# Kernel tuning notes

Hardware: AMD Instinct MI355X
Metric: run time of the kernel (lower is better)

The kernel has to match this reference:

```python
import jax, jax.numpy as jnp
from jax import lax
import numpy as np

C = 16          # channels
K = 3           # deformable kernel size
PAD = 1


def conv3(x, w, b):
    # 3x3 SAME conv, NCHW / OIHW
    y = lax.conv_general_dilated(x, w, (1, 1), 'SAME',
                                 dimension_numbers=('NCHW', 'OIHW', 'NCHW'))
    return y + b[None, :, None, None]


def deform_conv2d(x, offsets, mask, w, b):
    """torchvision-style modulated deformable conv, stride=1, pad=1, dil=1.
    x: [B,C,H,W]; offsets: [B,2*K*K,H,W] (per-tap y,x interleaved);
    mask: [B,K*K,H,W]; w: [Cout,C,K,K]; b: [Cout]."""
    B, Cin, H, W = x.shape
    ky, kx = jnp.meshgrid(jnp.arange(K), jnp.arange(K), indexing='ij')
    ky = ky.reshape(-1).astype(x.dtype)   # [9]
    kx = kx.reshape(-1).astype(x.dtype)
    off = offsets.reshape(B, K * K, 2, H, W)  # off[:,k,0]=dy, off[:,k,1]=dx
    hh = jnp.arange(H, dtype=x.dtype)
    ww = jnp.arange(W, dtype=x.dtype)
    py = hh[None, None, :, None] + (ky - PAD)[None, :, None, None] + off[:, :, 0]  # [B,9,H,W]
    px = ww[None, None, None, :] + (kx - PAD)[None, :, None, None] + off[:, :, 1]
    y0 = jnp.floor(py)
    x0 = jnp.floor(px)
    dy = py - y0
    dx = px - x0

    def sample_one(img, y0b, x0b, dyb, dxb):
        # img [C,H,W]; y0b/x0b/dyb/dxb [9,H,W]
        y0i = y0b.astype(jnp.int32)
        x0i = x0b.astype(jnp.int32)

        def gather(yi, xi):
            valid = ((yi >= 0) & (yi < H) & (xi >= 0) & (xi < W)).astype(img.dtype)
            yc = jnp.clip(yi, 0, H - 1)
            xc = jnp.clip(xi, 0, W - 1)
            return img[:, yc, xc] * valid[None]   # [C,9,H,W]

        v00 = gather(y0i,     x0i)
        v01 = gather(y0i,     x0i + 1)
        v10 = gather(y0i + 1, x0i)
        v11 = gather(y0i + 1, x0i + 1)
        return (v00 * (1 - dyb) * (1 - dxb) + v01 * (1 - dyb) * dxb
                + v10 * dyb * (1 - dxb) + v11 * dyb * dxb)   # [C,9,H,W]

    sampled = jax.vmap(sample_one)(x, y0, x0, dy, dx)          # [B,C,9,H,W]
    sampled = sampled * mask[:, None]                           # modulate
    out = jnp.einsum('bckhw,ock->bohw', sampled, w.reshape(w.shape[0], Cin, K * K))
    return out + b[None, :, None, None]


def setup_inputs() -> dict:
    key = jax.random.key(0)
    ks = iter(jax.random.split(key, 32))

    def w(shape, scale=0.1):
        return (jax.random.normal(next(ks), shape, dtype=jnp.float32) * scale)

    B, H, W = 4, 256, 256
    d = {
        'f_E': jax.random.normal(next(ks), (B, C, H, W), dtype=jnp.float32),
        'f_F': jax.random.normal(next(ks), (B, C, H, W), dtype=jnp.float32),
        # SpatialAttentionBlock
        'sab_att_w1': w((C, 2 * C, 3, 3)), 'sab_att_b1': w((C,)),
        'sab_att_w2': w((1, C, 3, 3)),      'sab_att_b2': w((1,)),
        'sab_ref_w':  w((C, 2 * C, 3, 3)),  'sab_ref_b':  w((C,)),
        # DeformableConvLayer offset/mask net (last layer small -> modest offsets)
        'om_w1': w((C, 2 * C, 3, 3)),       'om_b1': w((C,)),
        'om_w2': w((C, C, 3, 3)),           'om_b2': w((C,)),
        'om_w3': w((3 * K * K, C, 3, 3), 0.05), 'om_b3': w((3 * K * K,), 0.05),
        # deformable conv weight/bias
        'dcb_w': w((C, C, 3, 3)),           'dcb_b': w((C,)),
        # refinements
        'dcbref_w': w((C, 2 * C, 3, 3)),    'dcbref_b': w((C,)),
        'fin_w':    w((C, 2 * C, 3, 3)),    'fin_b':    w((C,)),
    }
    return d


def reference(f_E, f_F,
              sab_att_w1, sab_att_b1, sab_att_w2, sab_att_b2,
              sab_ref_w, sab_ref_b,
              om_w1, om_b1, om_w2, om_b2, om_w3, om_b3,
              dcb_w, dcb_b, dcbref_w, dcbref_b, fin_w, fin_b):
    relu = jax.nn.relu
    # --- SAB branch: sab(f_E, f_F) ---
    comb = jnp.concatenate([f_E, f_F], axis=1)
    M_E = jax.nn.sigmoid(conv3(relu(conv3(comb, sab_att_w1, sab_att_b1)),
                               sab_att_w2, sab_att_b2))          # [B,1,H,W]
    f_Esa = f_E * M_E
    f_EFsa = relu(conv3(jnp.concatenate([f_Esa, f_F], axis=1), sab_ref_w, sab_ref_b))
    # --- DCB branch: dcb_layer(f_F, f_E) -> deform on f_E, cat([f_E, f_F]) ---
    comb2 = jnp.concatenate([f_E, f_F], axis=1)
    om = conv3(relu(conv3(relu(conv3(comb2, om_w1, om_b1)), om_w2, om_b2)),
               om_w3, om_b3)                                      # [B,27,H,W]
    offsets = om[:, :2 * K * K]
    mask = jax.nn.sigmoid(om[:, 2 * K * K:])
    f_Edc = relu(deform_conv2d(f_E, offsets, mask, dcb_w, dcb_b))
    f_EFdc = relu(conv3(jnp.concatenate([f_Edc, f_F], axis=1), dcbref_w, dcbref_b))
    # --- final fusion ---
    f_EF = relu(conv3(jnp.concatenate([f_EFsa, f_EFdc], axis=1), fin_w, fin_b))
    return f_EF
```

## Files before the change

kernel.cpp:

```cpp
#include <hip/hip_runtime.h>
#include <cstdint>
#include <cstddef>

#define HH 256
#define WW 256
#define HWW (HH * WW)

typedef __attribute__((ext_vector_type(8))) short bf16x8;
typedef __attribute__((ext_vector_type(4))) float f32x4;

__device__ inline unsigned short f2bf(float f) {
  unsigned u = __float_as_uint(f);
  unsigned r = (u + 0x7fffu + ((u >> 16) & 1u)) >> 16;
  return (unsigned short)r;
}
__device__ inline float bf2f(unsigned short u) {
  return __uint_as_float((unsigned)u << 16);
}
__device__ inline float bf_lo(unsigned w) { return __uint_as_float(w << 16); }
__device__ inline float bf_hi(unsigned w) { return __uint_as_float(w & 0xffff0000u); }

struct RD { const float* src; void* dst; int cin, cout, mode; };
struct RA { RD d[9]; };

__device__ void repack_one(const RD& t) {
  if (t.mode == 2) {
    const int NST = (t.cin * 9 + 31) / 32;
    const int OT = (t.cout + 15) / 16;
    const int n = OT * NST * 512;
    unsigned short* dst = (unsigned short*)t.dst;
    for (int i = threadIdx.x; i < n; i += 256) {
      int j = i & 7;
      int l = (i >> 3) & 63;
      int rest = i >> 9;
      int s = rest % NST;
      int ot = rest / NST;
      int o = ot * 16 + (l & 15);
      int klin = s * 32 + ((l >> 4) << 3) + j;
      int tap = klin / t.cin;
      int c = klin % t.cin;
      float v = 0.f;
      if (tap < 9 && o < t.cout) v = t.src[(o * t.cin + c) * 9 + tap];
      dst[i] = f2bf(v);
    }
  } else {
    float* dst = (float*)t.dst;
    const int n = t.cin * t.cout * 9;
    for (int i = threadIdx.x; i < n; i += 256) {
      int k = i % 9;
      int rest = i / 9;
      int c = rest % t.cin;
      int o = rest / t.cin;
      if (t.mode == 0) dst[(c * 9 + k) * t.cout + o] = t.src[(o * t.cin + c) * 9 + k];
      else             dst[(k * t.cin + c) * t.cout + o] = t.src[(o * t.cin + c) * 9 + k];
    }
  }
}

__global__ __launch_bounds__(256) void prep_k(
    RA ra, const float* __restrict__ fe, const float* __restrict__ ff,
    unsigned short* __restrict__ xe, unsigned short* __restrict__ xf) {
  const int b = blockIdx.z;
  if (blockIdx.x == 256) {
    const int d0 = b * 3;
    for (int d = d0; d < d0 + 3 && d < 9; ++d) repack_one(ra.d[d]);
    return;
  }
  const int pixel = blockIdx.x * 256 + threadIdx.x;
#pragma unroll
  for (int t = 0; t < 2; ++t) {
    const float* src = t ? ff : fe;
    unsigned short* dst = t ? xf : xe;
    unsigned w[8];
#pragma unroll
    for (int j = 0; j < 8; ++j) {
      unsigned short lo = f2bf(src[((size_t)b * 16 + 2 * j) * HWW + pixel]);
      unsigned short hi = f2bf(src[((size_t)b * 16 + 2 * j + 1) * HWW + pixel]);
      w[j] = (unsigned)lo | ((unsigned)hi << 16);
    }
    uint4* d4 = (uint4*)(dst + ((size_t)b * HWW + pixel) * 16);
    d4[0] = make_uint4(w[0], w[1], w[2], w[3]);
    d4[1] = make_uint4(w[4], w[5], w[6], w[7]);
  }
}

__global__ __launch_bounds__(256) void conv_dual_k(
    const unsigned short* __restrict__ inA, const unsigned short* __restrict__ inB,
    const unsigned short* __restrict__ w1, const float* __restrict__ b1,
    const unsigned short* __restrict__ w2, const float* __restrict__ b2,
    unsigned short* __restrict__ out1, unsigned short* __restrict__ out2) {
  constexpr int NSLOT = 4, NST = 9, SHIFT = 1, STRIDE = 64, PX = 34, PY = 10;
  __shared__ __align__(16) char smem[PY * PX * STRIDE];

  const int b = blockIdx.z;
  const int tx0 = blockIdx.x * 32;
  const int ty0 = blockIdx.y * 8;
  const int tid = threadIdx.x;
  const int lane = tid & 63;
  const int wv = tid >> 6;

  bf16x8 afr1[NST], afr2[NST];
#pragma unroll
  for (int s = 0; s < NST; ++s) {
    afr1[s] = *(const bf16x8*)(w1 + (size_t)((s * 64 + lane) * 8));
    afr2[s] = *(const bf16x8*)(w2 + (size_t)((s * 64 + lane) * 8));
  }

  const int px_l = lane & 15;
  const int og = lane >> 4;

  f32x4 acc1[4], acc2[4];
  {
    f32x4 bv1, bv2;
#pragma unroll
    for (int r = 0; r < 4; ++r) {
      bv1[r] = b1[og * 4 + r];
      bv2[r] = b2[og * 4 + r];
    }
#pragma unroll
    for (int t = 0; t < 4; ++t) { acc1[t] = bv1; acc2[t] = bv2; }
  }

  for (int i = tid; i < PY * PX * NSLOT; i += 256) {
    int pp = i / NSLOT;
    int s = i - pp * NSLOT;
    int ly = pp / PX;
    int lx = pp - ly * PX;
    int gy = ty0 + ly - 1;
    int gx = tx0 + lx - 1;
    uint4 v = make_uint4(0, 0, 0, 0);
    if (gy >= 0 && gy < HH && gx >= 0 && gx < WW) {
      const unsigned short* src = (s < 2) ? inA : inB;
      int sl = (s >= 2) ? s - 2 : s;
      v = *(const uint4*)(src + ((size_t)b * HWW + (size_t)gy * WW + gx) * 16 + sl * 8);
    }
    int swz = (s ^ (pp >> SHIFT)) & 3;
    *(uint4*)(smem + (size_t)pp * STRIDE + (swz << 4)) = v;
  }
  __syncthreads();

  int dpix[NST], dslot[NST];
#pragma unroll
  for (int s = 0; s < NST; ++s) {
    int klin = s * 32 + og * 8;
    int tap = klin / 32;
    int coff = klin % 32;
    dpix[s] = (tap / 3) * PX + (tap % 3);
    dslot[s] = coff >> 3;
  }

  const int oy_l = wv * 2;
#pragma unroll
  for (int t = 0; t < 4; ++t) {
    const int base_pix = (oy_l + (t >> 1)) * PX + (t & 1) * 16 + px_l;
#pragma unroll
    for (int s = 0; s < NST; ++s) {
      int pp = base_pix + dpix[s];
      int off = pp * STRIDE + (((dslot[s] ^ (pp >> SHIFT)) & 3) << 4);
      bf16x8 bvv = *(const bf16x8*)(smem + off);
      acc1[t] = __builtin_amdgcn_mfma_f32_16x16x32_bf16(afr1[s], bvv, acc1[t], 0, 0, 0);
      acc2[t] = __builtin_amdgcn_mfma_f32_16x16x32_bf16(afr2[s], bvv, acc2[t], 0, 0, 0);
    }
  }

#pragma unroll
  for (int t = 0; t < 4; ++t) {
    const int gy = ty0 + oy_l + (t >> 1);
    const int gx = tx0 + (t & 1) * 16 + px_l;
    const size_t base = ((size_t)b * HWW + (size_t)gy * WW + gx) * 16 + og * 4;
    {
      unsigned lo = (unsigned)f2bf(fmaxf(acc1[t][0], 0.f)) |
                    ((unsigned)f2bf(fmaxf(acc1[t][1], 0.f)) << 16);
      unsigned hi = (unsigned)f2bf(fmaxf(acc1[t][2], 0.f)) |
                    ((unsigned)f2bf(fmaxf(acc1[t][3], 0.f)) << 16);
      *(uint2*)(out1 + base) = make_uint2(lo, hi);
    }
    {
      unsigned lo = (unsigned)f2bf(fmaxf(acc2[t][0], 0.f)) |
                    ((unsigned)f2bf(fmaxf(acc2[t][1], 0.f)) << 16);
      unsigned hi = (unsigned)f2bf(fmaxf(acc2[t][2], 0.f)) |
                    ((unsigned)f2bf(fmaxf(acc2[t][3], 0.f)) << 16);
      *(uint2*)(out2 + base) = make_uint2(lo, hi);
    }
  }
}

__global__ __launch_bounds__(256) void sagate_k(
    const unsigned short* __restrict__ xa, const unsigned short* __restrict__ xe,
    const unsigned short* __restrict__ xf,
    const float* __restrict__ gw, const float* __restrict__ gb,
    const unsigned short* __restrict__ wtm, const float* __restrict__ bias,
    unsigned short* __restrict__ out) {
  constexpr int NST = 9, SHIFT = 1, STRIDE = 64, PX = 34, PY = 10;
  __shared__ __align__(16) char smem[PY * PX * STRIDE];

  const int b = blockIdx.z;
  const int tx0 = blockIdx.x * 32;
  const int ty0 = blockIdx.y * 8;
  const int tid = threadIdx.x;
  const int lane = tid & 63;
  const int wv = tid >> 6;

  bf16x8 afr[NST];
#pragma unroll
  for (int s = 0; s < NST; ++s)
    afr[s] = *(const bf16x8*)(wtm + (size_t)((s * 64 + lane) * 8));

  const int px_l = lane & 15;
  const int og = lane >> 4;

  f32x4 acc[4];
  {
    f32x4 bv;
#pragma unroll
    for (int r = 0; r < 4; ++r) bv[r] = bias[og * 4 + r];
#pragma unroll
    for (int t = 0; t < 4; ++t) acc[t] = bv;
  }

  for (int i = tid; i < PY * PX * 2; i += 256) {
    int pp = i >> 1;
    int s = 2 + (i & 1);
    int ly = pp / PX;
    int lx = pp - ly * PX;
    int gy = ty0 + ly - 1;
    int gx = tx0 + lx - 1;
    uint4 v = make_uint4(0, 0, 0, 0);
    if (gy >= 0 && gy < HH && gx >= 0 && gx < WW)
      v = *(const uint4*)(xf + ((size_t)b * HWW + (size_t)gy * WW + gx) * 16 + (s - 2) * 8);
    int swz = (s ^ (pp >> SHIFT)) & 3;
    *(uint4*)(smem + (size_t)pp * STRIDE + (swz << 4)) = v;
  }

  const float gbias = gb[0];
  for (int i = tid; i < PY * PX; i += 256) {
    int ly = i / PX;
    int lx = i - ly * PX;
    int gy = ty0 + ly - 1;
    int gx = tx0 + lx - 1;
    uint4 v0 = make_uint4(0, 0, 0, 0), v1 = make_uint4(0, 0, 0, 0);
    if (gy >= 0 && gy < HH && gx >= 0 && gx < WW) {
      float a = gbias;
#pragma unroll
      for (int ky = 0; ky < 3; ++ky) {
        int ay = gy + ky - 1;
        if (ay < 0 || ay >= HH) continue;
#pragma unroll
        for (int kx = 0; kx < 3; ++kx) {
          int ax = gx + kx - 1;
          if (ax < 0 || ax >= WW) continue;
          const int k = ky * 3 + kx;
          const uint4* p = (const uint4*)(xa + ((size_t)b * HWW + (size_t)ay * WW + ax) * 16);
          uint4 t0 = p[0], t1 = p[1];
          unsigned wv8[8] = {t0.x, t0.y, t0.z, t0.w, t1.x, t1.y, t1.z, t1.w};
#pragma unroll
          for (int j = 0; j < 8; ++j) {
            a = fmaf(bf_lo(wv8[j]), gw[(2 * j) * 9 + k], a);
            a = fmaf(bf_hi(wv8[j]), gw[(2 * j + 1) * 9 + k], a);
          }
        }
      }
      float m = 1.0f / (1.0f + expf(-a));
      const uint4* pe = (const uint4*)(xe + ((size_t)b * HWW + (size_t)gy * WW + gx) * 16);
      uint4 e0 = pe[0], e1 = pe[1];
      unsigned ev[8] = {e0.x, e0.y, e0.z, e0.w, e1.x, e1.y, e1.z, e1.w};
      unsigned r[8];
#pragma unroll
      for (int j = 0; j < 8; ++j) {
        unsigned short lo = f2bf(bf_lo(ev[j]) * m);
        unsigned short hi = f2bf(bf_hi(ev[j]) * m);
        r[j] = (unsigned)lo | ((unsigned)hi << 16);
      }
      v0 = make_uint4(r[0], r[1], r[2], r[3]);
      v1 = make_uint4(r[4], r[5], r[6], r[7]);
    }
    int swz0 = (0 ^ (i >> SHIFT)) & 3;
    int swz1 = (1 ^ (i >> SHIFT)) & 3;
    *(uint4*)(smem + (size_t)i * STRIDE + (swz0 << 4)) = v0;
    *(uint4*)(smem + (size_t)i * STRIDE + (swz1 << 4)) = v1;
  }
  __syncthreads();

  int dpix[NST], dslot[NST];
#pragma unroll
  for (int s = 0; s < NST; ++s) {
    int klin = s * 32 + og * 8;
    int tap = klin / 32;
    int coff = klin % 32;
    dpix[s] = (tap / 3) * PX + (tap % 3);
    dslot[s] = coff >> 3;
  }

  const int oy_l = wv * 2;
#pragma unroll
  for (int t = 0; t < 4; ++t) {
    const int base_pix = (oy_l + (t >> 1)) * PX + (t & 1) * 16 + px_l;
#pragma unroll
    for (int s = 0; s < NST; ++s) {
      int pp = base_pix + dpix[s];
      int off = pp * STRIDE + (((dslot[s] ^ (pp >> SHIFT)) & 3) << 4);
      bf16x8 bvv = *(const bf16x8*)(smem + off);
      acc[t] = __builtin_amdgcn_mfma_f32_16x16x32_bf16(afr[s], bvv, acc[t], 0, 0, 0);
    }
  }

#pragma unroll
  for (int t = 0; t < 4; ++t) {
    const int gy = ty0 + oy_l + (t >> 1);
    const int gx = tx0 + (t & 1) * 16 + px_l;
    unsigned lo = (unsigned)f2bf(fmaxf(acc[t][0], 0.f)) |
                  ((unsigned)f2bf(fmaxf(acc[t][1], 0.f)) << 16);
    unsigned hi = (unsigned)f2bf(fmaxf(acc[t][2], 0.f)) |
                  ((unsigned)f2bf(fmaxf(acc[t][3], 0.f)) << 16);
    *(uint2*)(out + ((size_t)b * HWW + (size_t)gy * WW + gx) * 16 + og * 4) = make_uint2(lo, hi);
  }
}

__global__ __launch_bounds__(256) void om_fused_k(
    const unsigned short* __restrict__ xt,
    const unsigned short* __restrict__ w2m, const float* __restrict__ b2,
    const unsigned short* __restrict__ w3m, const float* __restrict__ b3,
    unsigned short* __restrict__ omb) {
  __shared__ __align__(16) char smem[12 * 36 * 32 + 10 * 34 * 32];
  char* stage = smem;
  char* t3 = smem + 12 * 36 * 32;

  const int b = blockIdx.z;
  const int tx0 = blockIdx.x * 32;
  const int ty0 = blockIdx.y * 8;
  const int tid = threadIdx.x;
  const int lane = tid & 63;
  const int wv = tid >> 6;
  const int px_l = lane & 15;
  const int og = lane >> 4;

  for (int i = tid; i < 12 * 36 * 2; i += 256) {
    int pp = i >> 1;
    int s = i & 1;
    int lr = pp / 36;
    int lc = pp - lr * 36;
    int gy = ty0 + lr - 2;
    int gx = tx0 + lc - 2;
    uint4 v = make_uint4(0, 0, 0, 0);
    if (gy >= 0 && gy < HH && gx >= 0 && gx < WW)
      v = *(const uint4*)(xt + ((size_t)b * HWW + (size_t)gy * WW + gx) * 16 + s * 8);
    int swz = (s ^ (pp >> 2)) & 1;
    *(uint4*)(stage + (size_t)pp * 32 + (swz << 4)) = v;
  }
  __syncthreads();

  {
    bf16x8 afr1[5];
#pragma unroll
    for (int s = 0; s < 5; ++s)
      afr1[s] = *(const bf16x8*)(w2m + (size_t)((s * 64 + lane) * 8));
    f32x4 bvec;
#pragma unroll
    for (int r = 0; r < 4; ++r) bvec[r] = b2[og * 4 + r];
    int tap1[5], slot1[5];
#pragma unroll
    for (int s = 0; s < 5; ++s) {
      int klin = s * 32 + og * 8;
      int tap = klin / 16;
      if (tap > 8) tap = 8;
      int coff = klin % 16;
      tap1[s] = (tap / 3) * 36 + (tap % 3);
      slot1[s] = coff >> 3;
    }
    for (int f = wv; f < 22; f += 4) {
      int p = f * 16 + px_l;
      int r = p / 34;
      int c = p - r * 34;
      f32x4 acc = bvec;
#pragma unroll
      for (int s = 0; s < 5; ++s) {
        int pp2 = r * 36 + c + tap1[s];
        int off = pp2 * 32 + (((slot1[s] ^ (pp2 >> 2)) & 1) << 4);
        bf16x8 bv = *(const bf16x8*)(stage + off);
        acc = __builtin_amdgcn_mfma_f32_16x16x32_bf16(afr1[s], bv, acc, 0, 0, 0);
      }
      if (p < 340) {
        int gy = ty0 + r - 1;
        int gx = tx0 + c - 1;
        unsigned lo = 0, hi = 0;
        if (gy >= 0 && gy < HH && gx >= 0 && gx < WW) {
          lo = (unsigned)f2bf(fmaxf(acc[0], 0.f)) | ((unsigned)f2bf(fmaxf(acc[1], 0.f)) << 16);
          hi = (unsigned)f2bf(fmaxf(acc[2], 0.f)) | ((unsigned)f2bf(fmaxf(acc[3], 0.f)) << 16);
        }
        int slot = og >> 1;
        int off = p * 32 + (((slot ^ (p >> 2)) & 1) << 4) + (og & 1) * 8;
        *(uint2*)(t3 + off) = make_uint2(lo, hi);
      }
    }
  }
  __syncthreads();

  bf16x8 afr2[2][5];
#pragma unroll
  for (int ot = 0; ot < 2; ++ot)
#pragma unroll
    for (int s = 0; s < 5; ++s)
      afr2[ot][s] = *(const bf16x8*)(w3m + (size_t)(((ot * 5 + s) * 64 + lane) * 8));

  f32x4 acc2[4][2];
#pragma unroll
  for (int ot = 0; ot < 2; ++ot) {
    f32x4 bv;
#pragma unroll
    for (int r = 0; r < 4; ++r) {
      int o = ot * 16 + og * 4 + r;
      bv[r] = b3[o < 27 ? o : 26];
    }
#pragma unroll
    for (int t = 0; t < 4; ++t) acc2[t][ot] = bv;
  }

  int tap2[5], slot2[5];
#pragma unroll
  for (int s = 0; s < 5; ++s) {
    int klin = s * 32 + og * 8;
    int tap = klin / 16;
    if (tap > 8) tap = 8;
    int coff = klin % 16;
    tap2[s] = (tap / 3) * 34 + (tap % 3);
    slot2[s] = coff >> 3;
  }

  const int oy_l = wv * 2;
#pragma unroll
  for (int t = 0; t < 4; ++t) {
    const int base_pix = (oy_l + (t >> 1)) * 34 + (t & 1) * 16 + px_l;
#pragma unroll
    for (int s = 0; s < 5; ++s) {
      int pp = base_pix + tap2[s];
      int off = pp * 32 + (((slot2[s] ^ (pp >> 2)) & 1) << 4);
      bf16x8 bv = *(const bf16x8*)(t3 + off);
      acc2[t][0] = __builtin_amdgcn_mfma_f32_16x16x32_bf16(afr2[0][s], bv, acc2[t][0], 0, 0, 0);
      acc2[t][1] = __builtin_amdgcn_mfma_f32_16x16x32_bf16(afr2[1][s], bv, acc2[t][1], 0, 0, 0);
    }
  }

#pragma unroll
  for (int t = 0; t < 4; ++t) {
    const int gy = ty0 + oy_l + (t >> 1);
    const int gx = tx0 + (t & 1) * 16 + px_l;
#pragma unroll
    for (int ot = 0; ot < 2; ++ot) {
      const int o0 = ot * 16 + og * 4;
#pragma unroll
      for (int r = 0; r < 4; ++r) {
        int o = o0 + r;
        if (o < 27)
          omb[((size_t)b * 27 + o) * HWW + (size_t)gy * WW + gx] = f2bf(acc2[t][ot][r]);
      }
    }
  }
}

__global__ __launch_bounds__(256) void deform_v4(
    const unsigned short* __restrict__ xn, const unsigned short* __restrict__ om,
    const float* __restrict__ wt, const float* __restrict__ bias,
    unsigned short* __restrict__ out) {
  const int bid = blockIdx.x;
  const int xcd = bid & 7;
  const int b = xcd >> 1;
  const int pb = ((bid >> 3) << 1) | (xcd & 1);
  const int pixel = pb * 256 + (int)threadIdx.x;
  const int y = pixel >> 8;
  const int xq = pixel & 255;
  const unsigned short* xb = xn + (size_t)b * HWW * 16;
  const unsigned short* omb = om + (size_t)b * 27 * HWW;

  float acc[16];
#pragma unroll
  for (int o = 0; o < 16; ++o) acc[o] = bias[o];

#pragma unroll
  for (int k = 0; k < 9; ++k) {
    float offy = bf2f(omb[(size_t)(2 * k) * HWW + pixel]);
    float offx = bf2f(omb[(size_t)(2 * k + 1) * HWW + pixel]);
    float m = 1.0f / (1.0f + expf(-bf2f(omb[(size_t)(18 + k) * HWW + pixel])));
    float py = (float)y + (float)(k / 3 - 1) + offy;
    float px = (float)xq + (float)(k % 3 - 1) + offx;
    float y0f = floorf(py);
    float x0f = floorf(px);
    float dy = py - y0f;
    float dx = px - x0f;
    int y0 = (int)y0f, x0 = (int)x0f;
    int y1 = y0 + 1, x1 = x0 + 1;
    bool vy0 = (y0 >= 0) && (y0 < HH);
    bool vy1 = (y1 >= 0) && (y1 < HH);
    bool vx0 = (x0 >= 0) && (x0 < WW);
    bool vx1 = (x1 >= 0) && (x1 < WW);
    int yc0 = min(max(y0, 0), HH - 1);
    int yc1 = min(max(y1, 0), HH - 1);
    int xc0 = min(max(x0, 0), WW - 1);
    int xc1 = min(max(x1, 0), WW - 1);
    float w00 = (1.f - dy) * (1.f - dx) * m;
    float w01 = (1.f - dy) * dx * m;
    float w10 = dy * (1.f - dx) * m;
    float w11 = dy * dx * m;
    if (!(vy0 && vx0)) w00 = 0.f;
    if (!(vy0 && vx1)) w01 = 0.f;
    if (!(vy1 && vx0)) w10 = 0.f;
    if (!(vy1 && vx1)) w11 = 0.f;

    const uint4* p00 = (const uint4*)(xb + (size_t)(yc0 * WW + xc0) * 16);
    const uint4* p01 = (const uint4*)(xb + (size_t)(yc0 * WW + xc1) * 16);
    const uint4* p10 = (const uint4*)(xb + (size_t)(yc1 * WW + xc0) * 16);
    const uint4* p11 = (const uint4*)(xb + (size_t)(yc1 * WW + xc1) * 16);
    uint4 a0 = p00[0], a1 = p00[1];
    uint4 b0 = p01[0], b1 = p01[1];
    uint4 c0 = p10[0], c1 = p10[1];
    uint4 d0 = p11[0], d1 = p11[1];
    unsigned wA[8] = {a0.x, a0.y, a0.z, a0.w, a1.x, a1.y, a1.z, a1.w};
    unsigned wB[8] = {b0.x, b0.y, b0.z, b0.w, b1.x, b1.y, b1.z, b1.w};
    unsigned wC[8] = {c0.x, c0.y, c0.z, c0.w, c1.x, c1.y, c1.z, c1.w};
    unsigned wD[8] = {d0.x, d0.y, d0.z, d0.w, d1.x, d1.y, d1.z, d1.w};

    float s[16];
#pragma unroll
    for (int j = 0; j < 8; ++j) {
      s[2 * j]     = bf_lo(wA[j]) * w00 + bf_lo(wB[j]) * w01 + bf_lo(wC[j]) * w10 + bf_lo(wD[j]) * w11;
      s[2 * j + 1] = bf_hi(wA[j]) * w00 + bf_hi(wB[j]) * w01 + bf_hi(wC[j]) * w10 + bf_hi(wD[j]) * w11;
    }
    const float* wk = wt + (size_t)k * 256;
#pragma unroll
    for (int c = 0; c < 16; ++c)
#pragma unroll
      for (int o = 0; o < 16; ++o)
        acc[o] = fmaf(s[c], wk[c * 16 + o], acc[o]);
  }
  unsigned r[8];
#pragma unroll
  for (int j = 0; j < 8; ++j) {
    unsigned short lo = f2bf(fmaxf(acc[2 * j], 0.f));
    unsigned short hi = f2bf(fmaxf(acc[2 * j + 1], 0.f));
    r[j] = (unsigned)lo | ((unsigned)hi << 16);
  }
  uint4* d4 = (uint4*)(out + ((size_t)b * HWW + pixel) * 16);
  d4[0] = make_uint4(r[0], r[1], r[2], r[3]);
  d4[1] = make_uint4(r[4], r[5], r[6], r[7]);
}

__global__ __launch_bounds__(256) void fin_fused_k(
    const unsigned short* __restrict__ xsa, const unsigned short* __restrict__ xf,
    const unsigned short* __restrict__ wdm, const float* __restrict__ bd,
    const unsigned short* __restrict__ x2,
    const unsigned short* __restrict__ wfm, const float* __restrict__ bfv,
    float* __restrict__ outp) {
  __shared__ __align__(16) char smem[12 * 36 * 64 + 10 * 34 * 32];
  char* stage = smem;
  char* dtile = smem + 12 * 36 * 64;
  char* x2tile = smem;

  const int b = blockIdx.z;
  const int tx0 = blockIdx.x * 32;
  const int ty0 = blockIdx.y * 8;
  const int tid = threadIdx.x;
  const int lane = tid & 63;
  const int wv = tid >> 6;
  const int px_l = lane & 15;
  const int og = lane >> 4;

  for (int i = tid; i < 12 * 36 * 4; i += 256) {
    int pp = i >> 2;
    int s = i & 3;
    int lr = pp / 36;
    int lc = pp - lr * 36;
    int gy = ty0 + lr - 2;
    int gx = tx0 + lc - 2;
    uint4 v = make_uint4(0, 0, 0, 0);
    if (gy >= 0 && gy < HH && gx >= 0 && gx < WW) {
      const unsigned short* src = (s < 2) ? xsa : xf;
      int sl = (s >= 2) ? s - 2 : s;
      v = *(const uint4*)(src + ((size_t)b * HWW + (size_t)gy * WW + gx) * 16 + sl * 8);
    }
    int swz = (s ^ (pp >> 1)) & 3;
    *(uint4*)(stage + (size_t)pp * 64 + (swz << 4)) = v;
  }
  __syncthreads();

  {
    bf16x8 afr1[9];
#pragma unroll
    for (int s = 0; s < 9; ++s)
      afr1[s] = *(const bf16x8*)(wdm + (size_t)((s * 64 + lane) * 8));
    f32x4 bvec;
#pragma unroll
    for (int r = 0; r < 4; ++r) bvec[r] = bd[og * 4 + r];
    int tap1[9], slot1[9];
#pragma unroll
    for (int s = 0; s < 9; ++s) {
      int klin = s * 32 + og * 8;
      int tap = klin / 32;
      int coff = klin % 32;
      tap1[s] = (tap / 3) * 36 + (tap % 3);
      slot1[s] = coff >> 3;
    }
    for (int f = wv; f < 22; f += 4) {
      int p = f * 16 + px_l;
      int r = p / 34;
      int c = p - r * 34;
      f32x4 acc = bvec;
#pragma unroll
      for (int s = 0; s < 9; ++s) {
        int pp2 = r * 36 + c + tap1[s];
        int off = pp2 * 64 + (((slot1[s] ^ (pp2 >> 1)) & 3) << 4);
        bf16x8 bv = *(const bf16x8*)(stage + off);
        acc = __builtin_amdgcn_mfma_f32_16x16x32_bf16(afr1[s], bv, acc, 0, 0, 0);
      }
      if (p < 340) {
        int gy = ty0 + r - 1;
        int gx = tx0 + c - 1;
        unsigned lo = 0, hi = 0;
        if (gy >= 0 && gy < HH && gx >= 0 && gx < WW) {
          lo = (unsigned)f2bf(fmaxf(acc[0], 0.f)) | ((unsigned)f2bf(fmaxf(acc[1], 0.f)) << 16);
          hi = (unsigned)f2bf(fmaxf(acc[2], 0.f)) | ((unsigned)f2bf(fmaxf(acc[3], 0.f)) << 16);
        }
        int slot = og >> 1;
        int off = p * 32 + (((slot ^ (p >> 2)) & 1) << 4) + (og & 1) * 8;
        *(uint2*)(dtile + off) = make_uint2(lo, hi);
      }
    }
  }
  __syncthreads();

  for (int i = tid; i < 340 * 2; i += 256) {
    int pp = i >> 1;
    int s = i & 1;
    int r = pp / 34;
    int c = pp - r * 34;
    int gy = ty0 + r - 1;
    int gx = tx0 + c - 1;
    uint4 v = make_uint4(0, 0, 0, 0);
    if (gy >= 0 && gy < HH && gx >= 0 && gx < WW)
      v = *(const uint4*)(x2 + ((size_t)b * HWW + (size_t)gy * WW + gx) * 16 + s * 8);
    int swz = (s ^ (pp >> 2)) & 1;
    *(uint4*)(x2tile + (size_t)pp * 32 + (swz << 4)) = v;
  }
  __syncthreads();

  bf16x8 afr2[9];
#pragma unroll
  for (int s = 0; s < 9; ++s)
    afr2[s] = *(const bf16x8*)(wfm + (size_t)((s * 64 + lane) * 8));

  f32x4 acc2[4];
  {
    f32x4 bv;
#pragma unroll
    for (int r = 0; r < 4; ++r) bv[r] = bfv[og * 4 + r];
#pragma unroll
    for (int t = 0; t < 4; ++t) acc2[t] = bv;
  }

  int tap2[9], slot2[9];
#pragma unroll
  for (int s = 0; s < 9; ++s) {
    int klin = s * 32 + og * 8;
    int tap = klin / 32;
    int coff = klin % 32;
    tap2[s] = (tap / 3) * 34 + (tap % 3);
    slot2[s] = coff >> 3;
  }

  const int oy_l = wv * 2;
#pragma unroll
  for (int t = 0; t < 4; ++t) {
    const int base_pix = (oy_l + (t >> 1)) * 34 + (t & 1) * 16 + px_l;
#pragma unroll
    for (int s = 0; s < 9; ++s) {
      int pp = base_pix + tap2[s];
      const char* basep = (slot2[s] < 2) ? x2tile : dtile;
      int sl = slot2[s] & 1;
      int off = pp * 32 + (((sl ^ (pp >> 2)) & 1) << 4);
      bf16x8 bv = *(const bf16x8*)(basep + off);
      acc2[t] = __builtin_amdgcn_mfma_f32_16x16x32_bf16(afr2[s], bv, acc2[t], 0, 0, 0);
    }
  }

#pragma unroll
  for (int t = 0; t < 4; ++t) {
    const int gy = ty0 + oy_l + (t >> 1);
    const int gx = tx0 + (t & 1) * 16 + px_l;
    const int o0 = og * 4;
#pragma unroll
    for (int r = 0; r < 4; ++r)
      outp[((size_t)b * 16 + o0 + r) * HWW + (size_t)gy * WW + gx] = fmaxf(acc2[t][r], 0.f);
  }
}

extern "C" void kernel_launch(void* const* d_in, const int* in_sizes, int n_in,
                              void* d_out, int out_size, void* d_ws, size_t ws_size,
                              hipStream_t stream) {
  (void)in_sizes; (void)n_in; (void)out_size; (void)ws_size;
  const float* f_E = (const float*)d_in[0];
  const float* f_F = (const float*)d_in[1];
  const float* att_w1 = (const float*)d_in[2];
  const float* att_b1 = (const float*)d_in[3];
  const float* att_w2 = (const float*)d_in[4];
  const float* att_b2 = (const float*)d_in[5];
  const float* ref_w = (const float*)d_in[6];
  const float* ref_b = (const float*)d_in[7];
  const float* om_w1 = (const float*)d_in[8];
  const float* om_b1 = (const float*)d_in[9];
  const float* om_w2 = (const float*)d_in[10];
  const float* om_b2 = (const float*)d_in[11];
  const float* om_w3 = (const float*)d_in[12];
  const float* om_b3 = (const float*)d_in[13];
  const float* dcb_w = (const float*)d_in[14];
  const float* dcb_b = (const float*)d_in[15];
  const float* dcbref_w = (const float*)d_in[16];
  const float* dcbref_b = (const float*)d_in[17];
  const float* fin_w = (const float*)d_in[18];
  const float* fin_b = (const float*)d_in[19];
  float* outp = (float*)d_out;

  const size_t TN = (size_t)4 * HWW * 16;
  unsigned short* XE  = (unsigned short*)d_ws;
  unsigned short* XF  = XE + TN;
  unsigned short* XA  = XF + TN;
  unsigned short* XT  = XA + TN;
  unsigned short* X2  = XT + TN;
  unsigned short* XSA = X2 + TN;
  unsigned short* OMB = XSA + TN;
  unsigned short* WM  = OMB + (size_t)4 * 27 * HWW;

  unsigned short* WM_att1 = WM;
  unsigned short* WM_ref  = WM_att1 + 4608;
  unsigned short* WM_om1  = WM_ref + 4608;
  unsigned short* WM_om2  = WM_om1 + 4608;
  unsigned short* WM_om3  = WM_om2 + 2560;
  unsigned short* WM_dref = WM_om3 + 5120;
  unsigned short* WM_fin  = WM_dref + 4608;
  float* WF_att2 = (float*)(WM_fin + 4608);
  float* WF_dcb  = WF_att2 + 144;

  RA ra;
  ra.d[0] = {att_w1, WM_att1, 32, 16, 2};
  ra.d[1] = {ref_w, WM_ref, 32, 16, 2};
  ra.d[2] = {om_w1, WM_om1, 32, 16, 2};
  ra.d[3] = {om_w2, WM_om2, 16, 16, 2};
  ra.d[4] = {om_w3, WM_om3, 16, 27, 2};
  ra.d[5] = {dcbref_w, WM_dref, 32, 16, 2};
  ra.d[6] = {fin_w, WM_fin, 32, 16, 2};
  ra.d[7] = {att_w2, WF_att2, 16, 1, 0};
  ra.d[8] = {dcb_w, WF_dcb, 16, 16, 1};

  dim3 blk(256);
  prep_k<<<dim3(257, 1, 4), blk, 0, stream>>>(ra, f_E, f_F, XE, XF);

  dim3 gm(WW / 32, HH / 8, 4);

  conv_dual_k<<<gm, blk, 0, stream>>>(XE, XF, WM_att1, att_b1, WM_om1, om_b1, XA, XT);
  sagate_k<<<gm, blk, 0, stream>>>(XA, XE, XF, WF_att2, att_b2, WM_ref, ref_b, X2);
  om_fused_k<<<gm, blk, 0, stream>>>(XT, WM_om2, om_b2, WM_om3, om_b3, OMB);
  deform_v4<<<dim3(1024), blk, 0, stream>>>(XE, OMB, WF_dcb, dcb_b, XSA);
  fin_fused_k<<<gm, blk, 0, stream>>>(XSA, XF, WM_dref, dcbref_b, X2, WM_fin, fin_b, outp);
}
```

Measured before the change: 109.2 us.

## Merge SA-gate and offset-mask kernels into one launch; split deform outputs across threads

The independent sagate and om_fused kernels are merged into one 2048-block launch, with even blocks doing the SA gate and refine conv and odd blocks doing the offset/mask convs. This removes a launch and lets the two branches run concurrently on the GPU. The deformable conv kernel now uses two threads per pixel, each computing 8 of the 16 output channels. That doubles parallelism and lowers per-thread register pressure, but each bilinear gather is now done by two threads. The merged kernel uses the larger shared memory footprint for both halves, which may reduce occupancy.

Result: slower. 172.0 us (+57.5%).

```diff
diff --git a/kernel.cpp b/kernel.cpp
--- a/kernel.cpp
+++ b/kernel.cpp
@@ -185,295 +185,291 @@
   }
 }
 
-__global__ __launch_bounds__(256) void sagate_k(
+__global__ __launch_bounds__(256) void mid_k(
     const unsigned short* __restrict__ xa, const unsigned short* __restrict__ xe,
     const unsigned short* __restrict__ xf,
     const float* __restrict__ gw, const float* __restrict__ gb,
-    const unsigned short* __restrict__ wtm, const float* __restrict__ bias,
-    unsigned short* __restrict__ out) {
-  constexpr int NST = 9, SHIFT = 1, STRIDE = 64, PX = 34, PY = 10;
-  __shared__ __align__(16) char smem[PY * PX * STRIDE];
-
-  const int b = blockIdx.z;
-  const int tx0 = blockIdx.x * 32;
-  const int ty0 = blockIdx.y * 8;
-  const int tid = threadIdx.x;
-  const int lane = tid & 63;
-  const int wv = tid >> 6;
-
-  bf16x8 afr[NST];
-#pragma unroll
-  for (int s = 0; s < NST; ++s)
-    afr[s] = *(const bf16x8*)(wtm + (size_t)((s * 64 + lane) * 8));
-
-  const int px_l = lane & 15;
-  const int og = lane >> 4;
-
-  f32x4 acc[4];
-  {
-    f32x4 bv;
-#pragma unroll
-    for (int r = 0; r < 4; ++r) bv[r] = bias[og * 4 + r];
-#pragma unroll
-    for (int t = 0; t < 4; ++t) acc[t] = bv;
-  }
-
-  for (int i = tid; i < PY * PX * 2; i += 256) {
-    int pp = i >> 1;
-    int s = 2 + (i & 1);
-    int ly = pp / PX;
-    int lx = pp - ly * PX;
-    int gy = ty0 + ly - 1;
-    int gx = tx0 + lx - 1;
-    uint4 v = make_uint4(0, 0, 0, 0);
-    if (gy >= 0 && gy < HH && gx >= 0 && gx < WW)
-      v = *(const uint4*)(xf + ((size_t)b * HWW + (size_t)gy * WW + gx) * 16 + (s - 2) * 8);
-    int swz = (s ^ (pp >> SHIFT)) & 3;
-    *(uint4*)(smem + (size_t)pp * STRIDE + (swz << 4)) = v;
-  }
-
-  const float gbias = gb[0];
-  for (int i = tid; i < PY * PX; i += 256) {
-    int ly = i / PX;
-    int lx = i - ly * PX;
-    int gy = ty0 + ly - 1;
-    int gx = tx0 + lx - 1;
-    uint4 v0 = make_uint4(0, 0, 0, 0), v1 = make_uint4(0, 0, 0, 0);
-    if (gy >= 0 && gy < HH && gx >= 0 && gx < WW) {
-      float a = gbias;
-#pragma unroll
-      for (int ky = 0; ky < 3; ++ky) {
-        int ay = gy + ky - 1;
-        if (ay < 0 || ay >= HH) continue;
-#pragma unroll
-        for (int kx = 0; kx < 3; ++kx) {
-          int ax = gx + kx - 1;
-          if (ax < 0 || ax >= WW) continue;
-          const int k = ky * 3 + kx;
-          const uint4* p = (const uint4*)(xa + ((size_t)b * HWW + (size_t)ay * WW + ax) * 16);
-          uint4 t0 = p[0], t1 = p[1];
-          unsigned wv8[8] = {t0.x, t0.y, t0.z, t0.w, t1.x, t1.y, t1.z, t1.w};
-#pragma unroll
-          for (int j = 0; j < 8; ++j) {
-            a = fmaf(bf_lo(wv8[j]), gw[(2 * j) * 9 + k], a);
-            a = fmaf(bf_hi(wv8[j]), gw[(2 * j + 1) * 9 + k], a);
-          }
-        }
-      }
-      float m = 1.0f / (1.0f + expf(-a));
-      const uint4* pe = (const uint4*)(xe + ((size_t)b * HWW + (size_t)gy * WW + gx) * 16);
-      uint4 e0 = pe[0], e1 = pe[1];
-      unsigned ev[8] = {e0.x, e0.y, e0.z, e0.w, e1.x, e1.y, e1.z, e1.w};
-      unsigned r[8];
-#pragma unroll
-      for (int j = 0; j < 8; ++j) {
-        unsigned short lo = f2bf(bf_lo(ev[j]) * m);
-        unsigned short hi = f2bf(bf_hi(ev[j]) * m);
-        r[j] = (unsigned)lo | ((unsigned)hi << 16);
-      }
-      v0 = make_uint4(r[0], r[1], r[2], r[3]);
-      v1 = make_uint4(r[4], r[5], r[6], r[7]);
-    }
-    int swz0 = (0 ^ (i >> SHIFT)) & 3;
-    int swz1 = (1 ^ (i >> SHIFT)) & 3;
-    *(uint4*)(smem + (size_t)i * STRIDE + (swz0 << 4)) = v0;
-    *(uint4*)(smem + (size_t)i * STRIDE + (swz1 << 4)) = v1;
-  }
-  __syncthreads();
-
-  int dpix[NST], dslot[NST];
-#pragma unroll
-  for (int s = 0; s < NST; ++s) {
-    int klin = s * 32 + og * 8;
-    int tap = klin / 32;
-    int coff = klin % 32;
-    dpix[s] = (tap / 3) * PX + (tap % 3);
-    dslot[s] = coff >> 3;
-  }
-
-  const int oy_l = wv * 2;
-#pragma unroll
-  for (int t = 0; t < 4; ++t) {
-    const int base_pix = (oy_l + (t >> 1)) * PX + (t & 1) * 16 + px_l;
-#pragma unroll
-    for (int s = 0; s < NST; ++s) {
-      int pp = base_pix + dpix[s];
-      int off = pp * STRIDE + (((dslot[s] ^ (pp >> SHIFT)) & 3) << 4);
-      bf16x8 bvv = *(const bf16x8*)(smem + off);
-      acc[t] = __builtin_amdgcn_mfma_f32_16x16x32_bf16(afr[s], bvv, acc[t], 0, 0, 0);
-    }
-  }
-
-#pragma unroll
-  for (int t = 0; t < 4; ++t) {
-    const int gy = ty0 + oy_l + (t >> 1);
-    const int gx = tx0 + (t & 1) * 16 + px_l;
-    unsigned lo = (unsigned)f2bf(fmaxf(acc[t][0], 0.f)) |
-                  ((unsigned)f2bf(fmaxf(acc[t][1], 0.f)) << 16);
-    unsigned hi = (unsigned)f2bf(fmaxf(acc[t][2], 0.f)) |
-                  ((unsigned)f2bf(fmaxf(acc[t][3], 0.f)) << 16);
-    *(uint2*)(out + ((size_t)b * HWW + (size_t)gy * WW + gx) * 16 + og * 4) = make_uint2(lo, hi);
-  }
-}
-
-__global__ __launch_bounds__(256) void om_fused_k(
+    const unsigned short* __restrict__ wrm, const float* __restrict__ rb,
+    unsigned short* __restrict__ x2out,
     const unsigned short* __restrict__ xt,
     const unsigned short* __restrict__ w2m, const float* __restrict__ b2,
     const unsigned short* __restrict__ w3m, const float* __restrict__ b3,
     unsigned short* __restrict__ omb) {
-  __shared__ __align__(16) char smem[12 * 36 * 32 + 10 * 34 * 32];
-  char* stage = smem;
-  char* t3 = smem + 12 * 36 * 32;
-
-  const int b = blockIdx.z;
-  const int tx0 = blockIdx.x * 32;
-  const int ty0 = blockIdx.y * 8;
+  __shared__ __align__(16) char smem[24704];
+
+  const int flat = blockIdx.x;
+  const int half = flat & 1;
+  const int rem = flat >> 1;
+  const int b = rem >> 8;
+  const int ty0 = ((rem >> 3) & 31) * 8;
+  const int tx0 = (rem & 7) * 32;
   const int tid = threadIdx.x;
   const int lane = tid & 63;
   const int wv = tid >> 6;
   const int px_l = lane & 15;
   const int og = lane >> 4;
 
-  for (int i = tid; i < 12 * 36 * 2; i += 256) {
-    int pp = i >> 1;
-    int s = i & 1;
-    int lr = pp / 36;
-    int lc = pp - lr * 36;
-    int gy = ty0 + lr - 2;
-    int gx = tx0 + lc - 2;
-    uint4 v = make_uint4(0, 0, 0, 0);
-    if (gy >= 0 && gy < HH && gx >= 0 && gx < WW)
-      v = *(const uint4*)(xt + ((size_t)b * HWW + (size_t)gy * WW + gx) * 16 + s * 8);
-    int swz = (s ^ (pp >> 2)) & 1;
-    *(uint4*)(stage + (size_t)pp * 32 + (swz << 4)) = v;
-  }
-  __syncthreads();
-
-  {
-    bf16x8 afr1[5];
-#pragma unroll
-    for (int s = 0; s < 5; ++s)
-      afr1[s] = *(const bf16x8*)(w2m + (size_t)((s * 64 + lane) * 8));
-    f32x4 bvec;
-#pragma unroll
-    for (int r = 0; r < 4; ++r) bvec[r] = b2[og * 4 + r];
-    int tap1[5], slot1[5];
+  if (half == 0) {
+    constexpr int NST = 9, SHIFT = 1, STRIDE = 64, PX = 34, PY = 10;
+    bf16x8 afr[NST];
+#pragma unroll
+    for (int s = 0; s < NST; ++s)
+      afr[s] = *(const bf16x8*)(wrm + (size_t)((s * 64 + lane) * 8));
+
+    f32x4 acc[4];
+    {
+      f32x4 bv;
+#pragma unroll
+      for (int r = 0; r < 4; ++r) bv[r] = rb[og * 4 + r];
+#pragma unroll
+      for (int t = 0; t < 4; ++t) acc[t] = bv;
+    }
+
+    for (int i = tid; i < PY * PX * 2; i += 256) {
+      int pp = i >> 1;
+      int s = 2 + (i & 1);
+      int ly = pp / PX;
+      int lx = pp - ly * PX;
+      int gy = ty0 + ly - 1;
+      int gx = tx0 + lx - 1;
+      uint4 v = make_uint4(0, 0, 0, 0);
+      if (gy >= 0 && gy < HH && gx >= 0 && gx < WW)
+        v = *(const uint4*)(xf + ((size_t)b * HWW + (size_t)gy * WW + gx) * 16 + (s - 2) * 8);
+      int swz = (s ^ (pp >> SHIFT)) & 3;
+      *(uint4*)(smem + (size_t)pp * STRIDE + (swz << 4)) = v;
+    }
+
+    const float gbias = gb[0];
+    for (int i = tid; i < PY * PX; i += 256) {
+      int ly = i / PX;
+      int lx = i - ly * PX;
+      int gy = ty0 + ly - 1;
+      int gx = tx0 + lx - 1;
+      uint4 v0 = make_uint4(0, 0, 0, 0), v1 = make_uint4(0, 0, 0, 0);
+      if (gy >= 0 && gy < HH && gx >= 0 && gx < WW) {
+        float a = gbias;
+#pragma unroll
+        for (int ky = 0; ky < 3; ++ky) {
+          int ay = gy + ky - 1;
+          if (ay < 0 || ay >= HH) continue;
+#pragma unroll
+          for (int kx = 0; kx < 3; ++kx) {
+            int ax = gx + kx - 1;
+            if (ax < 0 || ax >= WW) continue;
+            const int k = ky * 3 + kx;
+            const uint4* p = (const uint4*)(xa + ((size_t)b * HWW + (size_t)ay * WW + ax) * 16);
+            uint4 t0 = p[0], t1 = p[1];
+            unsigned wv8[8] = {t0.x, t0.y, t0.z, t0.w, t1.x, t1.y, t1.z, t1.w};
+#pragma unroll
+            for (int j = 0; j < 8; ++j) {
+              a = fmaf(bf_lo(wv8[j]), gw[(2 * j) * 9 + k], a);
+              a = fmaf(bf_hi(wv8[j]), gw[(2 * j + 1) * 9 + k], a);
+            }
+          }
+        }
+        float m = 1.0f / (1.0f + expf(-a));
+        const uint4* pe = (const uint4*)(xe + ((size_t)b * HWW + (size_t)gy * WW + gx) * 16);
+        uint4 e0 = pe[0], e1 = pe[1];
+        unsigned ev[8] = {e0.x, e0.y, e0.z, e0.w, e1.x, e1.y, e1.z, e1.w};
+        unsigned r[8];
+#pragma unroll
+        for (int j = 0; j < 8; ++j) {
+          unsigned short lo = f2bf(bf_lo(ev[j]) * m);
+          unsigned short hi = f2bf(bf_hi(ev[j]) * m);
+          r[j] = (unsigned)lo | ((unsigned)hi << 16);
+        }
+        v0 = make_uint4(r[0], r[1], r[2], r[3]);
+        v1 = make_uint4(r[4], r[5], r[6], r[7]);
+      }
+      int swz0 = (0 ^ (i >> SHIFT)) & 3;
+      int swz1 = (1 ^ (i >> SHIFT)) & 3;
+      *(uint4*)(smem + (size_t)i * STRIDE + (swz0 << 4)) = v0;
+      *(uint4*)(smem + (size_t)i * STRIDE + (swz1 << 4)) = v1;
+    }
+    __syncthreads();
+
+    int dpix[NST], dslot[NST];
+#pragma unroll
+    for (int s = 0; s < NST; ++s) {
+      int klin = s * 32 + og * 8;
+      int tap = klin / 32;
+      int coff = klin % 32;
+      dpix[s] = (tap / 3) * PX + (tap % 3);
+      dslot[s] = coff >> 3;
+    }
+
+    const int oy_l = wv * 2;
+#pragma unroll
+    for (int t = 0; t < 4; ++t) {
+      const int base_pix = (oy_l + (t >> 1)) * PX + (t & 1) * 16 + px_l;
+#pragma unroll
+      for (int s = 0; s < NST; ++s) {
+        int pp = base_pix + dpix[s];
+        int off = pp * STRIDE + (((dslot[s] ^ (pp >> SHIFT)) & 3) << 4);
+        bf16x8 bvv = *(const bf16x8*)(smem + off);
+        acc[t] = __builtin_amdgcn_mfma_f32_16x16x32_bf16(afr[s], bvv, acc[t], 0, 0, 0);
+      }
+    }
+
+#pragma unroll
+    for (int t = 0; t < 4; ++t) {
+      const int gy = ty0 + oy_l + (t >> 1);
+      const int gx = tx0 + (t & 1) * 16 + px_l;
+      unsigned lo = (unsigned)f2bf(fmaxf(acc[t][0], 0.f)) |
+                    ((unsigned)f2bf(fmaxf(acc[t][1], 0.f)) << 16);
+      unsigned hi = (unsigned)f2bf(fmaxf(acc[t][2], 0.f)) |
+                    ((unsigned)f2bf(fmaxf(acc[t][3], 0.f)) << 16);
+      *(uint2*)(x2out + ((size_t)b * HWW + (size_t)gy * WW + gx) * 16 + og * 4) = make_uint2(lo, hi);
+    }
+  } else {
+    char* stage = smem;
+    char* t3 = smem + 12 * 36 * 32;
+
+    for (int i = tid; i < 12 * 36 * 2; i += 256) {
+      int pp = i >> 1;
+      int s = i & 1;
+      int lr = pp / 36;
+      int lc = pp - lr * 36;
+      int gy = ty0 + lr - 2;
+      int gx = tx0 + lc - 2;
+      uint4 v = make_uint4(0, 0, 0, 0);
+      if (gy >= 0 && gy < HH && gx >= 0 && gx < WW)
+        v = *(const uint4*)(xt + ((size_t)b * HWW + (size_t)gy * WW + gx) * 16 + s * 8);
+      int swz = (s ^ (pp >> 2)) & 1;
+      *(uint4*)(stage + (size_t)pp * 32 + (swz << 4)) = v;
+    }
+    __syncthreads();
+
+    {
+      bf16x8 afr1[5];
+#pragma unroll
+      for (int s = 0; s < 5; ++s)
+        afr1[s] = *(const bf16x8*)(w2m + (size_t)((s * 64 + lane) * 8));
+      f32x4 bvec;
+#pragma unroll
+      for (int r = 0; r < 4; ++r) bvec[r] = b2[og * 4 + r];
+      int tap1[5], slot1[5];
+#pragma unroll
+      for (int s = 0; s < 5; ++s) {
+        int klin = s * 32 + og * 8;
+        int tap = klin / 16;
+        if (tap > 8) tap = 8;
+        int coff = klin % 16;
+        tap1[s] = (tap / 3) * 36 + (tap % 3);
+        slot1[s] = coff >> 3;
+      }
+      for (int f = wv; f < 22; f += 4) {
+        int p = f * 16 + px_l;
+        int r = p / 34;
+        int c = p - r * 34;
+        f32x4 acc = bvec;
+#pragma unroll
+        for (int s = 0; s < 5; ++s) {
+          int pp2 = r * 36 + c + tap1[s];
+          int off = pp2 * 32 + (((slot1[s] ^ (pp2 >> 2)) & 1) << 4);
+          bf16x8 bv = *(const bf16x8*)(stage + off);
+          acc = __builtin_amdgcn_mfma_f32_16x16x32_bf16(afr1[s], bv, acc, 0, 0, 0);
+        }
+        if (p < 340) {
+          int gy = ty0 + r - 1;
+          int gx = tx0 + c - 1;
+          unsigned lo = 0, hi = 0;
+          if (gy >= 0 && gy < HH && gx >= 0 && gx < WW) {
+            lo = (unsigned)f2bf(fmaxf(acc[0], 0.f)) | ((unsigned)f2bf(fmaxf(acc[1], 0.f)) << 16);
+            hi = (unsigned)f2bf(fmaxf(acc[2], 0.f)) | ((unsigned)f2bf(fmaxf(acc[3], 0.f)) << 16);
+          }
+          int slot = og >> 1;
+          int off = p * 32 + (((slot ^ (p >> 2)) & 1) << 4) + (og & 1) * 8;
+          *(uint2*)(t3 + off) = make_uint2(lo, hi);
+        }
+      }
+    }
+    __syncthreads();
+
+    bf16x8 afr2[2][5];
+#pragma unroll
+    for (int ot = 0; ot < 2; ++ot)
+#pragma unroll
+      for (int s = 0; s < 5; ++s)
+        afr2[ot][s] = *(const bf16x8*)(w3m + (size_t)(((ot * 5 + s) * 64 + lane) * 8));
+
+    f32x4 acc2[4][2];
+#pragma unroll
+    for (int ot = 0; ot < 2; ++ot) {
+      f32x4 bv;
+#pragma unroll
+      for (int r = 0; r < 4; ++r) {
+        int o = ot * 16 + og * 4 + r;
+        bv[r] = b3[o < 27 ? o : 26];
+      }
+#pragma unroll
+      for (int t = 0; t < 4; ++t) acc2[t][ot] = bv;
+    }
+
+    int tap2[5], slot2[5];
 #pragma unroll
     for (int s = 0; s < 5; ++s) {
       int klin = s * 32 + og * 8;
       int tap = klin / 16;
       if (tap > 8) tap = 8;
       int coff = klin % 16;
-      tap1[s] = (tap / 3) * 36 + (tap % 3);
-      slot1[s] = coff >> 3;
-    }
-    for (int f = wv; f < 22; f += 4) {
-      int p = f * 16 + px_l;
-      int r = p / 34;
-      int c = p - r * 34;
-      f32x4 acc = bvec;
+      tap2[s] = (tap / 3) * 34 + (tap % 3);
+      slot2[s] = coff >> 3;
+    }
+
+    const int oy_l = wv * 2;
+#pragma unroll
+    for (int t = 0; t < 4; ++t) {
+      const int base_pix = (oy_l + (t >> 1)) * 34 + (t & 1) * 16 + px_l;
 #pragma unroll
       for (int s = 0; s < 5; ++s) {
-        int pp2 = r * 36 + c + tap1[s];
-        int off = pp2 * 32 + (((slot1[s] ^ (pp2 >> 2)) & 1) << 4);
-        bf16x8 bv = *(const bf16x8*)(stage + off);
-        acc = __builtin_amdgcn_mfma_f32_16x16x32_bf16(afr1[s], bv, acc, 0, 0, 0);
-      }
-      if (p < 340) {
-        int gy = ty0 + r - 1;
-        int gx = tx0 + c - 1;
-        unsigned lo = 0, hi = 0;
-        if (gy >= 0 && gy < HH && gx >= 0 && gx < WW) {
-          lo = (unsigned)f2bf(fmaxf(acc[0], 0.f)) | ((unsigned)f2bf(fmaxf(acc[1], 0.f)) << 16);
-          hi = (unsigned)f2bf(fmaxf(acc[2], 0.f)) | ((unsigned)f2bf(fmaxf(acc[3], 0.f)) << 16);
+        int pp = base_pix + tap2[s];
+        int off = pp * 32 + (((slot2[s] ^ (pp >> 2)) & 1) << 4);
+        bf16x8 bv = *(const bf16x8*)(t3 + off);
+        acc2[t][0] = __builtin_amdgcn_mfma_f32_16x16x32_bf16(afr2[0][s], bv, acc2[t][0], 0, 0, 0);
+        acc2[t][1] = __builtin_amdgcn_mfma_f32_16x16x32_bf16(afr2[1][s], bv, acc2[t][1], 0, 0, 0);
+      }
+    }
+
+#pragma unroll
+    for (int t = 0; t < 4; ++t) {
+      const int gy = ty0 + oy_l + (t >> 1);
+      const int gx = tx0 + (t & 1) * 16 + px_l;
+#pragma unroll
+      for (int ot = 0; ot < 2; ++ot) {
+        const int o0 = ot * 16 + og * 4;
+#pragma unroll
+        for (int r = 0; r < 4; ++r) {
+          int o = o0 + r;
+          if (o < 27)
+            omb[((size_t)b * 27 + o) * HWW + (size_t)gy * WW + gx] = f2bf(acc2[t][ot][r]);
         }
-        int slot = og >> 1;
-        int off = p * 32 + (((slot ^ (p >> 2)) & 1) << 4) + (og & 1) * 8;
-        *(uint2*)(t3 + off) = make_uint2(lo, hi);
-      }
-    }
-  }
-  __syncthreads();
-
-  bf16x8 afr2[2][5];
-#pragma unroll
-  for (int ot = 0; ot < 2; ++ot)
-#pragma unroll
-    for (int s = 0; s < 5; ++s)
-      afr2[ot][s] = *(const bf16x8*)(w3m + (size_t)(((ot * 5 + s) * 64 + lane) * 8));
-
-  f32x4 acc2[4][2];
-#pragma unroll
-  for (int ot = 0; ot < 2; ++ot) {
-    f32x4 bv;
-#pragma unroll
-    for (int r = 0; r < 4; ++r) {
-      int o = ot * 16 + og * 4 + r;
-      bv[r] = b3[o < 27 ? o : 26];
-    }
-#pragma unroll
-    for (int t = 0; t < 4; ++t) acc2[t][ot] = bv;
-  }
-
-  int tap2[5], slot2[5];
-#pragma unroll
-  for (int s = 0; s < 5; ++s) {
-    int klin = s * 32 + og * 8;
-    int tap = klin / 16;
-    if (tap > 8) tap = 8;
-    int coff = klin % 16;
-    tap2[s] = (tap / 3) * 34 + (tap % 3);
-    slot2[s] = coff >> 3;
-  }
-
-  const int oy_l = wv * 2;
-#pragma unroll
-  for (int t = 0; t < 4; ++t) {
-    const int base_pix = (oy_l + (t >> 1)) * 34 + (t & 1) * 16 + px_l;
-#pragma unroll
-    for (int s = 0; s < 5; ++s) {
-      int pp = base_pix + tap2[s];
-      int off = pp * 32 + (((slot2[s] ^ (pp >> 2)) & 1) << 4);
-      bf16x8 bv = *(const bf16x8*)(t3 + off);
-      acc2[t][0] = __builtin_amdgcn_mfma_f32_16x16x32_bf16(afr2[0][s], bv, acc2[t][0], 0, 0, 0);
-      acc2[t][1] = __builtin_amdgcn_mfma_f32_16x16x32_bf16(afr2[1][s], bv, acc2[t][1], 0, 0, 0);
-    }
-  }
-
-#pragma unroll
-  for (int t = 0; t < 4; ++t) {
-    const int gy = ty0 + oy_l + (t >> 1);
-    const int gx = tx0 + (t & 1) * 16 + px_l;
-#pragma unroll
-    for (int ot = 0; ot < 2; ++ot) {
-      const int o0 = ot * 16 + og * 4;
-#pragma unroll
-      for (int r = 0; r < 4; ++r) {
-        int o = o0 + r;
-        if (o < 27)
-          omb[((size_t)b * 27 + o) * HWW + (size_t)gy * WW + gx] = f2bf(acc2[t][ot][r]);
-      }
-    }
-  }
-}
-
-__global__ __launch_bounds__(256) void deform_v4(
+      }
+    }
+  }
+}
+
+__global__ __launch_bounds__(256) void deform_v5(
     const unsigned short* __restrict__ xn, const unsigned short* __restrict__ om,
     const float* __restrict__ wt, const float* __restrict__ bias,
     unsigned short* __restrict__ out) {
   const int bid = blockIdx.x;
   const int xcd = bid & 7;
   const int b = xcd >> 1;
-  const int pb = ((bid >> 3) << 1) | (xcd & 1);
-  const int pixel = pb * 256 + (int)threadIdx.x;
+  const int pg = ((bid >> 3) << 1) | (xcd & 1);
+  const int tid = threadIdx.x;
+  const int half = tid >> 7;
+  const int lpx = tid & 127;
+  const int pixel = pg * 128 + lpx;
   const int y = pixel >> 8;
   const int xq = pixel & 255;
   const unsigned short* xb = xn + (size_t)b * HWW * 16;
   const unsigned short* omb = om + (size_t)b * 27 * HWW;
-
-  float acc[16];
-#pragma unroll
-  for (int o = 0; o < 16; ++o) acc[o] = bias[o];
+  const int ob = half * 8;
+
+  float acc[8];
+#pragma unroll
+  for (int o = 0; o < 8; ++o) acc[o] = bias[ob + o];
 
 #pragma unroll
   for (int k = 0; k < 9; ++k) {
@@ -509,38 +505,41 @@
     const uint4* p01 = (const uint4*)(xb + (size_t)(yc0 * WW + xc1) * 16);
     const uint4* p10 = (const uint4*)(xb + (size_t)(yc1 * WW + xc0) * 16);
     const uint4* p11 = (const uint4*)(xb + (size_t)(yc1 * WW + xc1) * 16);
-    uint4 a0 = p00[0], a1 = p00[1];
-    uint4 b0 = p01[0], b1 = p01[1];
-    uint4 c0 = p10[0], c1 = p10[1];
-    uint4 d0 = p11[0], d1 = p11[1];
-    unsigned wA[8] = {a0.x, a0.y, a0.z, a0.w, a1.x, a1.y, a1.z, a1.w};
-    unsigned wB[8] = {b0.x, b0.y, b0.z, b0.w, b1.x, b1.y, b1.z, b1.w};
-    unsigned wC[8] = {c0.x, c0.y, c0.z, c0.w, c1.x, c1.y, c1.z, c1.w};
-    unsigned wD[8] = {d0.x, d0.y, d0.z, d0.w, d1.x, d1.y, d1.z, d1.w};
-
-    float s[16];
-#pragma unroll
-    for (int j = 0; j < 8; ++j) {
-      s[2 * j]     = bf_lo(wA[j]) * w00 + bf_lo(wB[j]) * w01 + bf_lo(wC[j]) * w10 + bf_lo(wD[j]) * w11;
-      s[2 * j + 1] = bf_hi(wA[j]) * w00 + bf_hi(wB[j]) * w01 + bf_hi(wC[j]) * w10 + bf_hi(wD[j]) * w11;
-    }
-    const float* wk = wt + (size_t)k * 256;
-#pragma unroll
-    for (int c = 0; c < 16; ++c)
-#pragma unroll
-      for (int o = 0; o < 16; ++o)
-        acc[o] = fmaf(s[c], wk[c * 16 + o], acc[o]);
-  }
-  unsigned r[8];
-#pragma unroll
-  for (int j = 0; j < 8; ++j) {
+    const float* wkb = wt + (size_t)k * 256 + ob;
+
+#pragma unroll
+    for (int j2 = 0; j2 < 2; ++j2) {
+      uint4 a0 = p00[j2];
+      uint4 b0 = p01[j2];
+      uint4 c0 = p10[j2];
+      uint4 d0 = p11[j2];
+      unsigned wA[4] = {a0.x, a0.y, a0.z, a0.w};
+      unsigned wB[4] = {b0.x, b0.y, b0.z, b0.w};
+      unsigned wC[4] = {c0.x, c0.y, c0.z, c0.w};
+      unsigned wD[4] = {d0.x, d0.y, d0.z, d0.w};
+      float s[8];
+#pragma unroll
+      for (int j = 0; j < 4; ++j) {
+        s[2 * j]     = bf_lo(wA[j]) * w00 + bf_lo(wB[j]) * w01 + bf_lo(wC[j]) * w10 + bf_lo(wD[j]) * w11;
+        s[2 * j + 1] = bf_hi(wA[j]) * w00 + bf_hi(wB[j]) * w01 + bf_hi(wC[j]) * w10 + bf_hi(wD[j]) * w11;
+      }
+#pragma unroll
+      for (int c8 = 0; c8 < 8; ++c8) {
+        const float* wr = wkb + (size_t)(j2 * 8 + c8) * 16;
+#pragma unroll
+        for (int o = 0; o < 8; ++o)
+          acc[o] = fmaf(s[c8], wr[o], acc[o]);
+      }
+    }
+  }
+  unsigned r[4];
+#pragma unroll
+  for (int j = 0; j < 4; ++j) {
     unsigned short lo = f2bf(fmaxf(acc[2 * j], 0.f));
     unsigned short hi = f2bf(fmaxf(acc[2 * j + 1], 0.f));
     r[j] = (unsigned)lo | ((unsigned)hi << 16);
   }
-  uint4* d4 = (uint4*)(out + ((size_t)b * HWW + pixel) * 16);
-  d4[0] = make_uint4(r[0], r[1], r[2], r[3]);
-  d4[1] = make_uint4(r[4], r[5], r[6], r[7]);
+  *(uint4*)(out + ((size_t)b * HWW + pixel) * 16 + ob) = make_uint4(r[0], r[1], r[2], r[3]);
 }
 
 __global__ __launch_bounds__(256) void fin_fused_k(
@@ -754,8 +753,8 @@
   dim3 gm(WW / 32, HH / 8, 4);
 
   conv_dual_k<<<gm, blk, 0, stream>>>(XE, XF, WM_att1, att_b1, WM_om1, om_b1, XA, XT);
-  sagate_k<<<gm, blk, 0, stream>>>(XA, XE, XF, WF_att2, att_b2, WM_ref, ref_b, X2);
-  om_fused_k<<<gm, blk, 0, stream>>>(XT, WM_om2, om_b2, WM_om3, om_b3, OMB);
-  deform_v4<<<dim3(1024), blk, 0, stream>>>(XE, OMB, WF_dcb, dcb_b, XSA);
+  mid_k<<<dim3(2048), blk, 0, stream>>>(XA, XE, XF, WF_att2, att_b2, WM_ref, ref_b, X2,
+                                        XT, WM_om2, om_b2, WM_om3, om_b3, OMB);
+  deform_v5<<<dim3(2048), blk, 0, stream>>>(XE, OMB, WF_dcb, dcb_b, XSA);
   fin_fused_k<<<gm, blk, 0, stream>>>(XSA, XF, WM_dref, dcbref_b, X2, WM_fin, fin_b, outp);
 }
```
